# Optimization experiments

Hardware: AMD Instinct MI355X
Metric: run time of the kernel (lower is better)

The kernel has to match this reference:

```python
import jax, jax.numpy as jnp
import numpy as np

B, S, D_IN, D_OUT = 4, 2048, 1024, 1024

def setup_inputs() -> dict:
    key = jax.random.key(0)
    kx, kq, kk, kv = jax.random.split(key, 4)
    sc = 1.0 / np.sqrt(D_IN)
    x = jax.random.normal(kx, (B, S, D_IN), dtype=jnp.float32)
    Wq = jax.random.normal(kq, (D_IN, D_OUT), dtype=jnp.float32) * sc
    Wk = jax.random.normal(kk, (D_IN, D_OUT), dtype=jnp.float32) * sc
    Wv = jax.random.normal(kv, (D_IN, D_OUT), dtype=jnp.float32) * sc
    return {"x": x, "Wq": Wq, "Wk": Wk, "Wv": Wv}

def reference(x, Wq, Wk, Wv):
    # x: [B,S,Din]; projections to [B,S,Dout]
    q = jnp.einsum('bsd,de->bse', x, Wq)
    k = jnp.einsum('bsd,de->bse', x, Wk)
    v = jnp.einsum('bsd,de->bse', x, Wv)
    scale = 1.0 / jnp.sqrt(jnp.asarray(q.shape[-1], q.dtype))
    scores = jnp.einsum('bqe,bke->bqk', q, k) * scale  # [B,S,S]
    causal = jnp.tril(jnp.ones((scores.shape[-2], scores.shape[-1]), dtype=bool))
    scores = jnp.where(causal, scores, -jnp.inf)
    attn = jax.nn.softmax(scores, axis=-1)
    # dropout p=0.0 -> identity
    return jnp.einsum('bqk,bke->bqe', attn, v)
```

## Files before the change

### kernel.cpp

```cpp
#include <hip/hip_runtime.h>

#define SEQ 2048
#define DIM 1024

typedef __attribute__((ext_vector_type(8))) __bf16 bf16x8;
typedef __attribute__((ext_vector_type(4))) float f32x4;

typedef __attribute__((address_space(1))) unsigned char gu8_t;
typedef __attribute__((address_space(3))) unsigned char lu8_t;

__device__ __forceinline__ void async_copy16(const void* g, void* l) {
  __builtin_amdgcn_global_load_lds((gu8_t*)g, (lu8_t*)l, 16, 0, 0);
}

__device__ __forceinline__ ushort f2bf(float f) {
  union { float f; unsigned u; } v;
  v.f = f;
  unsigned r = v.u + 0x7FFFu + ((v.u >> 16) & 1u);
  return (ushort)(r >> 16);
}

__global__ void prep(const void* __restrict__ xin, const void* __restrict__ w0,
                     const void* __restrict__ w1, const void* __restrict__ w2,
                     ushort* __restrict__ xb, ushort* __restrict__ wt,
                     int* __restrict__ flag, float* __restrict__ lsum) {
  __shared__ ushort tile[64][68];
  __shared__ int redi[4];
  const int bid = blockIdx.x;
  const int t = threadIdx.x;

  const unsigned* words = (const unsigned*)xin;
  int hits = 0;
#pragma unroll
  for (int i = 0; i < 4; i++) {
    const unsigned wv = words[t * 4 + i];
    const unsigned b = (wv >> 8) & 0x7Fu;
    hits += (b >= 0x3Bu && b <= 0x42u) ? 1 : 0;
  }
#pragma unroll
  for (int o = 32; o > 0; o >>= 1) hits += __shfl_xor(hits, o, 64);
  if ((t & 63) == 0) redi[t >> 6] = hits;
  __syncthreads();
  const int bf = (redi[0] + redi[1] + redi[2] + redi[3] > 512) ? 1 : 0;

  if (bid >= 1792) {
    reinterpret_cast<float4*>(lsum)[(bid - 1792) * 256 + t] =
        make_float4(0.f, 0.f, 0.f, 0.f);
    if (bid == 1792 && t == 0) *flag = bf;
    return;
  }

  if (bid < 1024) {
#pragma unroll
    for (int j = 0; j < 4; j++) {
      const int i = bid * 1024 + j * 256 + t;
      if (bf) {
        reinterpret_cast<uint4*>(xb)[i] =
            reinterpret_cast<const uint4*>(xin)[i];
      } else {
        const float4* f = reinterpret_cast<const float4*>(xin);
        const float4 a = f[2 * i], b = f[2 * i + 1];
        ushort4 lo, hi;
        lo.x = f2bf(a.x); lo.y = f2bf(a.y); lo.z = f2bf(a.z); lo.w = f2bf(a.w);
        hi.x = f2bf(b.x); hi.y = f2bf(b.y); hi.z = f2bf(b.z); hi.w = f2bf(b.w);
        reinterpret_cast<ushort4*>(xb)[2 * i] = lo;
        reinterpret_cast<ushort4*>(xb)[2 * i + 1] = hi;
      }
    }
    return;
  }

  const int rem = bid - 1024;
  const int z = rem >> 8;
  const int within = rem & 255;
  const int c0 = (within & 15) * 64, r0 = (within >> 4) * 64;
  const void* in = (z == 0) ? w0 : (z == 1) ? w1 : w2;
  ushort* op = wt + (size_t)z * 1024 * 1024;

  if (bf) {
    const ushort* ip = (const ushort*)in;
#pragma unroll
    for (int i = 0; i < 4; i++) {
      const int lin = i * 256 + t;
      const int r = lin >> 4, c4 = (lin & 15) << 2;
      const ushort4 v = *reinterpret_cast<const ushort4*>(
          ip + (size_t)(r0 + r) * 1024 + c0 + c4);
      tile[r][c4 + 0] = v.x; tile[r][c4 + 1] = v.y;
      tile[r][c4 + 2] = v.z; tile[r][c4 + 3] = v.w;
    }
  } else {
    const float* ip = (const float*)in;
#pragma unroll
    for (int i = 0; i < 4; i++) {
      const int lin = i * 256 + t;
      const int r = lin >> 4, c4 = (lin & 15) << 2;
      const float4 v = *reinterpret_cast<const float4*>(
          ip + (size_t)(r0 + r) * 1024 + c0 + c4);
      tile[r][c4 + 0] = f2bf(v.x); tile[r][c4 + 1] = f2bf(v.y);
      tile[r][c4 + 2] = f2bf(v.z); tile[r][c4 + 3] = f2bf(v.w);
    }
  }
  __syncthreads();
#pragma unroll
  for (int i = 0; i < 4; i++) {
    const int lin = i * 256 + t;
    const int c = lin >> 4, r4 = (lin & 15) << 2;
    ushort4 v;
    v.x = tile[r4 + 0][c]; v.y = tile[r4 + 1][c];
    v.z = tile[r4 + 2][c]; v.w = tile[r4 + 3][c];
    *reinterpret_cast<ushort4*>(op + (size_t)(c0 + c) * 1024 + r0 + r4) = v;
  }
}

template <int MODE>
__global__ __launch_bounds__(512, 2) void gemm8(
    const ushort* __restrict__ p0, const ushort* __restrict__ p1,
    const ushort* __restrict__ p2, void* __restrict__ c0,
    void* __restrict__ c1, float* __restrict__ lsum) {
  __shared__ ushort sA[2][2][128 * 64];
  __shared__ ushort sB[2][2][128 * 64];

  const ushort* A;
  const ushort* B;
  ushort* C;
  float* ls = nullptr;
  int m0, n0;
  long ldA, ldB, ldC;
  float scale = 1.0f;
  bool isE = false;

  const int id = blockIdx.x;
  if constexpr (MODE == 0) {
    const int z = id >> 7, r = id & 127;
    m0 = (r >> 2) << 8;
    n0 = (r & 3) << 8;
    A = p0; ldA = 1024;
    B = p1 + (size_t)z * 1024 * 1024; ldB = 1024;
    C = (ushort*)c0 + (size_t)z * 8192 * 1024; ldC = 1024;
    scale = z ? 1.0f : 0.03125f;
  } else {
    if (id < 144) {
      isE = true;
      const int z = id / 36;
      const int tri = id % 36;
      int mt = 0;
      while ((mt + 1) * (mt + 2) / 2 <= tri) mt++;
      const int nt = tri - mt * (mt + 1) / 2;
      m0 = mt << 8;
      n0 = nt << 8;
      A = p0 + (size_t)z * SEQ * DIM; ldA = 1024;
      B = p0 + (size_t)8192 * 1024 + (size_t)z * SEQ * DIM; ldB = 1024;
      C = (ushort*)c0 + (size_t)z * SEQ * SEQ; ldC = 2048;
      ls = lsum + (size_t)z * SEQ;
    } else {
      const int r = id - 144;
      m0 = (r >> 5) << 8;
      n0 = (r & 31) << 8;
      A = p1 + 2 * 1024 * 1024; ldA = 1024;
      B = p2; ldB = 1024;
      C = (ushort*)c1; ldC = 8192;
    }
  }
  const int nT = 16;

  const int tid = threadIdx.x;
  const int lane = tid & 63;
  const int w = tid >> 6;
  const int quad = lane >> 4;
  const int l15 = lane & 15;
  const int ah = w >> 2;
  const int wn = (w & 3) << 6;
  const int bh = wn >> 7;
  const int bo = wn & 64;

  const ushort* aSrc[2][2];
  const ushort* bSrc[2][2];
#pragma unroll
  for (int h = 0; h < 2; h++)
#pragma unroll
    for (int i = 0; i < 2; i++) {
      const int g = i * 512 + tid;
      const int rl = g >> 3;
      const int ck = (g & 7) ^ (rl & 7);
      aSrc[h][i] = A + (size_t)(m0 + h * 128 + rl) * ldA + ck * 8;
      bSrc[h][i] = B + (size_t)(n0 + h * 128 + rl) * ldB + ck * 8;
    }

  auto stageA = [&](int t, int b) {
#pragma unroll
    for (int h = 0; h < 2; h++)
#pragma unroll
      for (int i = 0; i < 2; i++)
        async_copy16(aSrc[h][i] + t * 64, &sA[b][h][(i * 512 + tid) * 8]);
  };
  auto stageB = [&](int t, int b) {
#pragma unroll
    for (int h = 0; h < 2; h++)
#pragma unroll
      for (int i = 0; i < 2; i++)
        async_copy16(bSrc[h][i] + t * 64, &sB[b][h][(i * 512 + tid) * 8]);
  };
  auto rdA = [&](int b, int rbase, int kh) -> bf16x8 {
    const int row = rbase + l15;
    const int ck = ((kh << 2) | quad) ^ (row & 7);
    return *(const bf16x8*)&sA[b][ah][row * 64 + ck * 8];
  };
  auto rdB = [&](int b, int rbase, int kh) -> bf16x8 {
    const int row = rbase + l15;
    const int ck = ((kh << 2) | quad) ^ (row & 7);
    return *(const bf16x8*)&sB[b][bh][row * 64 + ck * 8];
  };

  f32x4 acc[8][4] = {};
  bf16x8 aF[8], bF0[4], bF1[4];

  stageA(0, 0); stageB(0, 0);
  stageA(1, 1); stageB(1, 1);
  asm volatile("s_waitcnt vmcnt(8)" ::: "memory");
  __builtin_amdgcn_s_barrier();

#pragma unroll 1
  for (int t = 0; t < nT; t++) {
    const int b = t & 1;

#pragma unroll
    for (int m = 0; m < 4; m++)
#pragma unroll
      for (int h = 0; h < 2; h++) aF[m * 2 + h] = rdA(b, m * 16, h);
#pragma unroll
    for (int n = 0; n < 2; n++)
#pragma unroll
      for (int h = 0; h < 2; h++) bF0[n * 2 + h] = rdB(b, bo + n * 16, h);
    __builtin_amdgcn_s_barrier();
    __builtin_amdgcn_s_setprio(1);
#pragma unroll
    for (int h = 0; h < 2; h++)
#pragma unroll
      for (int m = 0; m < 4; m++)
#pragma unroll
        for (int n = 0; n < 2; n++)
          acc[m][n] = __builtin_amdgcn_mfma_f32_16x16x32_bf16(
              aF[m * 2 + h], bF0[n * 2 + h], acc[m][n], 0, 0, 0);
    __builtin_amdgcn_s_setprio(0);
    __builtin_amdgcn_s_barrier();

#pragma unroll
    for (int n = 0; n < 2; n++)
#pragma unroll
      for (int h = 0; h < 2; h++)
        bF1[n * 2 + h] = rdB(b, bo + 32 + n * 16, h);
    __builtin_amdgcn_s_barrier();
    __builtin_amdgcn_s_setprio(1);
#pragma unroll
    for (int h = 0; h < 2; h++)
#pragma unroll
      for (int m = 0; m < 4; m++)
#pragma unroll
        for (int n = 0; n < 2; n++)
          acc[m][2 + n] = __builtin_amdgcn_mfma_f32_16x16x32_bf16(
              aF[m * 2 + h], bF1[n * 2 + h], acc[m][2 + n], 0, 0, 0);
    __builtin_amdgcn_s_setprio(0);
    __builtin_amdgcn_s_barrier();

#pragma unroll
    for (int m = 0; m < 4; m++)
#pragma unroll
      for (int h = 0; h < 2; h++) aF[m * 2 + h] = rdA(b, 64 + m * 16, h);
    if (t + 2 < nT) stageB(t + 2, b);
    __builtin_amdgcn_s_barrier();
    __builtin_amdgcn_s_setprio(1);
#pragma unroll
    for (int h = 0; h < 2; h++)
#pragma unroll
      for (int m = 0; m < 4; m++)
#pragma unroll
        for (int n = 0; n < 2; n++)
          acc[4 + m][n] = __builtin_amdgcn_mfma_f32_16x16x32_bf16(
              aF[m * 2 + h], bF0[n * 2 + h], acc[4 + m][n], 0, 0, 0);
    __builtin_amdgcn_s_setprio(0);
    __builtin_amdgcn_s_barrier();

    if (t + 2 < nT) stageA(t + 2, b);
    __builtin_amdgcn_s_setprio(1);
#pragma unroll
    for (int h = 0; h < 2; h++)
#pragma unroll
      for (int m = 0; m < 4; m++)
#pragma unroll
        for (int n = 0; n < 2; n++)
          acc[4 + m][2 + n] = __builtin_amdgcn_mfma_f32_16x16x32_bf16(
              aF[m * 2 + h], bF1[n * 2 + h], acc[4 + m][2 + n], 0, 0, 0);
    __builtin_amdgcn_s_setprio(0);
    if (t + 2 < nT)
      asm volatile("s_waitcnt vmcnt(8)" ::: "memory");
    else
      asm volatile("s_waitcnt vmcnt(0)" ::: "memory");
    __builtin_amdgcn_s_barrier();
  }

  if (MODE == 1 && isE) {
#pragma unroll
    for (int mi = 0; mi < 8; mi++)
#pragma unroll
      for (int r = 0; r < 4; r++) {
        const int row = m0 + ah * 128 + mi * 16 + quad * 4 + r;
        float partial = 0.0f;
#pragma unroll
        for (int ni = 0; ni < 4; ni++) {
          const int col = n0 + wn + ni * 16 + l15;
          const float ev = (col <= row) ? __expf(acc[mi][ni][r]) : 0.0f;
          C[(size_t)row * ldC + col] = f2bf(ev);
          partial += ev;
        }
#pragma unroll
        for (int o = 1; o < 16; o <<= 1) partial += __shfl_xor(partial, o, 64);
        if (l15 == 0) atomicAdd(&ls[row], partial);
      }
  } else {
#pragma unroll
    for (int mi = 0; mi < 8; mi++)
#pragma unroll
      for (int ni = 0; ni < 4; ni++)
#pragma unroll
        for (int r = 0; r < 4; r++) {
          const int row = m0 + ah * 128 + mi * 16 + quad * 4 + r;
          const int col = n0 + wn + ni * 16 + l15;
          C[(size_t)row * ldC + col] = f2bf(acc[mi][ni][r] * scale);
        }
  }
}

template <int EPI, int OUTK, int CK, int SWIZ, int M, int N, int K, long AZ,
          long BZ, long CZ, long BRS>
__global__ __launch_bounds__(256, 4) void gemm_t(
    const ushort* __restrict__ A, const ushort* __restrict__ Bt,
    void* __restrict__ Cv, const int* __restrict__ flag,
    float* __restrict__ lsum, float scale0, float scale1) {
  __shared__ ushort lA[128 * 64];
  __shared__ ushort lB[128 * 64];
  __shared__ float lsh[(EPI == 2) ? 128 : 1];

  constexpr int MT = M / 128;
  const int nT = gridDim.x;
  const int id = blockIdx.y * nT + blockIdx.x;
  const int xcd = id & 7;
  const int loc = id >> 3;
  int nt, mt;
  if constexpr (SWIZ == 1) {
    const int ng = nT >> 3;
    nt = xcd * ng + loc % ng;
    mt = loc / ng;
  } else if constexpr (SWIZ == 2) {
    if (loc <= xcd) { mt = xcd; nt = loc; }
    else { mt = MT - 1 - xcd; nt = loc - xcd - 1; }
  } else if constexpr (SWIZ == 3) {
    nt = xcd;
    mt = loc;
  } else {
    nt = loc % nT;
    mt = xcd + ((loc / nT) << 3);
  }
  const int n0 = nt * 128;
  const int m0 = mt * 128;

  const int z = blockIdx.z;
  const ushort* Ab = A + (size_t)z * AZ;
  const ushort* Bb = Bt + (size_t)z * BZ;

  const int t = threadIdx.x;
  const int lane = t & 63;
  const int w = t >> 6;
  const int wm = (w >> 1) * 64;
  const int wn = (w & 1) * 64;
  const int quad = lane >> 4;
  const int l15 = lane & 15;

  if constexpr (EPI == 2) {
    if (t < 128) lsh[t] = 1.0f / lsum[(size_t)z * M + m0 + t];
  }

  f32x4 acc[4][4] = {};

  const int kEnd = CK ? ((m0 + 128 < K) ? (m0 + 128) : K) : K;

  for (int k0 = 0; k0 < kEnd; k0 += 64) {
    __syncthreads();
#pragma unroll
    for (int g0 = 0; g0 < 1024; g0 += 256) {
      const int g = g0 + t;
      const int r = g >> 3, c = (g & 7) << 3;
      async_copy16(Ab + (size_t)(m0 + r) * K + k0 + c, lA + g * 8);
    }
#pragma unroll
    for (int g0 = 0; g0 < 1024; g0 += 256) {
      const int g = g0 + t;
      const int r = g >> 3, c = (g & 7) << 3;
      async_copy16(Bb + (size_t)(n0 + r) * BRS + k0 + c, lB + g * 8);
    }
    __syncthreads();

#pragma unroll
    for (int h = 0; h < 2; h++) {
      bf16x8 af[4], bfr[4];
#pragma unroll
      for (int mi = 0; mi < 4; mi++)
        af[mi] = *(const bf16x8*)(lA + (wm + mi * 16 + l15) * 64 + h * 32 +
                                  quad * 8);
#pragma unroll
      for (int ni = 0; ni < 4; ni++)
        bfr[ni] = *(const bf16x8*)(lB + (wn + ni * 16 + l15) * 64 + h * 32 +
                                   quad * 8);
#pragma unroll
      for (int mi = 0; mi < 4; mi++)
#pragma unroll
        for (int ni = 0; ni < 4; ni++)
          acc[mi][ni] = __builtin_amdgcn_mfma_f32_16x16x32_bf16(
              af[mi], bfr[ni], acc[mi][ni], 0, 0, 0);
    }
  }

  const size_t zc = (size_t)z * CZ;

  if constexpr (EPI == 1) {
    ushort* C = (ushort*)Cv + zc;
    float* ls = lsum + (size_t)z * M;
#pragma unroll
    for (int mi = 0; mi < 4; mi++)
#pragma unroll
      for (int r = 0; r < 4; r++) {
        const int row = m0 + wm + mi * 16 + quad * 4 + r;
        float partial = 0.0f;
#pragma unroll
        for (int ni = 0; ni < 4; ni++) {
          const int col = n0 + wn + ni * 16 + l15;
          const float ev = (col <= row) ? __expf(acc[mi][ni][r]) : 0.0f;
          C[(size_t)row * N + col] = f2bf(ev);
          partial += ev;
        }
#pragma unroll
        for (int o = 1; o < 16; o <<= 1) partial += __shfl_xor(partial, o, 64);
        if (l15 == 0) atomicAdd(&ls[row], partial);
      }
    return;
  } else {
    const float scale = (z == 0) ? scale0 : scale1;
    const bool storeBf = (OUTK == 1) || (OUTK == 2 && *flag != 0);
#pragma unroll
    for (int mi = 0; mi < 4; mi++)
#pragma unroll
      for (int ni = 0; ni < 4; ni++)
#pragma unroll
        for (int r = 0; r < 4; r++) {
          const int lrow = wm + mi * 16 + quad * 4 + r;
          const int row = m0 + lrow;
          const int col = n0 + wn + ni * 16 + l15;
          const float sc = (EPI == 2) ? lsh[lrow] : scale;
          const float vv = acc[mi][ni][r] * sc;
          if (storeBf) {
            ushort* C = (ushort*)Cv + zc;
            C[(size_t)row * N + col] = f2bf(vv);
          } else {
            float* C = (float*)Cv + zc;
            C[(size_t)row * N + col] = vv;
          }
        }
  }
}

extern "C" void kernel_launch(void* const* d_in, const int* in_sizes, int n_in,
                              void* d_out, int out_size, void* d_ws,
                              size_t ws_size, hipStream_t stream) {
  char* ws = (char*)d_ws;
  const size_t MB = 1024 * 1024;
  int* flag = (int*)ws;
  ushort* wt = (ushort*)(ws + 1 * MB);
  ushort* xb = (ushort*)(ws + 7 * MB);
  ushort* q = (ushort*)(ws + 23 * MB);
  ushort* vt = (ushort*)(ws + 55 * MB);
  ushort* sc = (ushort*)(ws + 71 * MB);
  float* lsum = (float*)(ws + 103 * MB);

  prep<<<dim3(1800), 256, 0, stream>>>(d_in[0], d_in[1], d_in[2], d_in[3], xb,
                                       wt, flag, lsum);

  gemm8<0><<<dim3(256), 512, 0, stream>>>(xb, wt, nullptr, (void*)q, nullptr,
                                          nullptr);

  gemm8<1><<<dim3(272), 512, 0, stream>>>(q, wt, xb, (void*)sc, (void*)vt,
                                          lsum);

  gemm_t<2, 2, 1, 3, 2048, 1024, 2048, (long)SEQ * SEQ, 2048L,
         (long)SEQ * DIM, 8192L>
      <<<dim3(8, 16, 4), 256, 0, stream>>>(sc, vt, d_out, flag, lsum, 1.0f,
                                           1.0f);
}
```

Measured before the change: 241.6 us.

## Replace P·V gemm with split-K 256x256 gemm8 mode using atomic fp32 accumulation

The final attention-times-V GEMM now runs on the larger pipelined 256x256 gemm8 kernel instead of the simpler 128x128 gemm_t. The causal K range is split into balanced chunks through a packed lookup table, giving 60 blocks per batch. Each block scales its partial result by the inverse row sum and atomically adds it into a zeroed fp32 output. This improves tile reuse and load balance across the triangular work, at the cost of an extra memset, atomic adds to global memory, and dropping the bf16 output path that the flag used to select.

```diff
diff --git a/kernel.cpp b/kernel.cpp
--- a/kernel.cpp
+++ b/kernel.cpp
@@ -122,10 +122,13 @@
 
   const ushort* A;
   const ushort* B;
-  ushort* C;
+  ushort* C = nullptr;
+  float* Cf = nullptr;
   float* ls = nullptr;
   int m0, n0;
-  long ldA, ldB, ldC;
+  int k0 = 0;
+  int nTloc = 16;
+  long ldA, ldB, ldC = 0;
   float scale = 1.0f;
   bool isE = false;
 
@@ -138,7 +141,7 @@
     B = p1 + (size_t)z * 1024 * 1024; ldB = 1024;
     C = (ushort*)c0 + (size_t)z * 8192 * 1024; ldC = 1024;
     scale = z ? 1.0f : 0.03125f;
-  } else {
+  } else if constexpr (MODE == 1) {
     if (id < 144) {
       isE = true;
       const int z = id / 36;
@@ -160,8 +163,26 @@
       B = p2; ldB = 1024;
       C = (ushort*)c1; ldC = 8192;
     }
-  }
-  const int nT = 16;
+  } else {
+    const int z = id / 60;
+    const int rr = id % 60;
+    const int nt = rr / 15;
+    const int u = rr % 15;
+    const unsigned long long lut0 = 0x855C845343824100ULL;
+    const unsigned long long lut1 = 0x00779F876E5E869DULL;
+    const unsigned bb =
+        (unsigned)((u < 8 ? (lut0 >> (8 * u)) : (lut1 >> (8 * (u - 8)))) &
+                   0xFFull);
+    const int mt = bb & 7;
+    k0 = ((bb >> 3) & 7) << 8;
+    nTloc = (int)((bb >> 6) + 1) << 2;
+    m0 = mt << 8;
+    n0 = nt << 8;
+    A = p0 + (size_t)z * SEQ * SEQ; ldA = 2048;
+    B = p1 + (size_t)z * SEQ; ldB = 8192;
+    Cf = (float*)c0 + (size_t)z * SEQ * DIM;
+    ls = lsum + (size_t)z * SEQ;
+  }
 
   const int tid = threadIdx.x;
   const int lane = tid & 63;
@@ -182,8 +203,8 @@
       const int g = i * 512 + tid;
       const int rl = g >> 3;
       const int ck = (g & 7) ^ (rl & 7);
-      aSrc[h][i] = A + (size_t)(m0 + h * 128 + rl) * ldA + ck * 8;
-      bSrc[h][i] = B + (size_t)(n0 + h * 128 + rl) * ldB + ck * 8;
+      aSrc[h][i] = A + (size_t)(m0 + h * 128 + rl) * ldA + k0 + ck * 8;
+      bSrc[h][i] = B + (size_t)(n0 + h * 128 + rl) * ldB + k0 + ck * 8;
     }
 
   auto stageA = [&](int t, int b) {
@@ -220,7 +241,7 @@
   __builtin_amdgcn_s_barrier();
 
 #pragma unroll 1
-  for (int t = 0; t < nT; t++) {
+  for (int t = 0; t < nTloc; t++) {
     const int b = t & 1;
 
 #pragma unroll
@@ -266,7 +287,7 @@
     for (int m = 0; m < 4; m++)
 #pragma unroll
       for (int h = 0; h < 2; h++) aF[m * 2 + h] = rdA(b, 64 + m * 16, h);
-    if (t + 2 < nT) stageB(t + 2, b);
+    if (t + 2 < nTloc) stageB(t + 2, b);
     __builtin_amdgcn_s_barrier();
     __builtin_amdgcn_s_setprio(1);
 #pragma unroll
@@ -280,7 +301,7 @@
     __builtin_amdgcn_s_setprio(0);
     __builtin_amdgcn_s_barrier();
 
-    if (t + 2 < nT) stageA(t + 2, b);
+    if (t + 2 < nTloc) stageA(t + 2, b);
     __builtin_amdgcn_s_setprio(1);
 #pragma unroll
     for (int h = 0; h < 2; h++)
@@ -291,11 +312,31 @@
           acc[4 + m][2 + n] = __builtin_amdgcn_mfma_f32_16x16x32_bf16(
               aF[m * 2 + h], bF1[n * 2 + h], acc[4 + m][2 + n], 0, 0, 0);
     __builtin_amdgcn_s_setprio(0);
-    if (t + 2 < nT)
+    if (t + 2 < nTloc)
       asm volatile("s_waitcnt vmcnt(8)" ::: "memory");
     else
       asm volatile("s_waitcnt vmcnt(0)" ::: "memory");
     __builtin_amdgcn_s_barrier();
+  }
+
+  if constexpr (MODE == 2) {
+    __syncthreads();
+    float* lshp = (float*)(&sA[0][0][0]);
+    if (tid < 256) lshp[tid] = 1.0f / ls[m0 + tid];
+    __syncthreads();
+#pragma unroll
+    for (int mi = 0; mi < 8; mi++)
+#pragma unroll
+      for (int ni = 0; ni < 4; ni++)
+#pragma unroll
+        for (int r = 0; r < 4; r++) {
+          const int rl_ = ah * 128 + mi * 16 + quad * 4 + r;
+          const int row = m0 + rl_;
+          const int col = n0 + wn + ni * 16 + l15;
+          atomicAdd(&Cf[(size_t)row * DIM + col],
+                    acc[mi][ni][r] * lshp[rl_]);
+        }
+    return;
   }
 
   if (MODE == 1 && isE) {
@@ -326,143 +367,6 @@
           const int row = m0 + ah * 128 + mi * 16 + quad * 4 + r;
           const int col = n0 + wn + ni * 16 + l15;
           C[(size_t)row * ldC + col] = f2bf(acc[mi][ni][r] * scale);
-        }
-  }
-}
-
-template <int EPI, int OUTK, int CK, int SWIZ, int M, int N, int K, long AZ,
-          long BZ, long CZ, long BRS>
-__global__ __launch_bounds__(256, 4) void gemm_t(
-    const ushort* __restrict__ A, const ushort* __restrict__ Bt,
-    void* __restrict__ Cv, const int* __restrict__ flag,
-    float* __restrict__ lsum, float scale0, float scale1) {
-  __shared__ ushort lA[128 * 64];
-  __shared__ ushort lB[128 * 64];
-  __shared__ float lsh[(EPI == 2) ? 128 : 1];
-
-  constexpr int MT = M / 128;
-  const int nT = gridDim.x;
-  const int id = blockIdx.y * nT + blockIdx.x;
-  const int xcd = id & 7;
-  const int loc = id >> 3;
-  int nt, mt;
-  if constexpr (SWIZ == 1) {
-    const int ng = nT >> 3;
-    nt = xcd * ng + loc % ng;
-    mt = loc / ng;
-  } else if constexpr (SWIZ == 2) {
-    if (loc <= xcd) { mt = xcd; nt = loc; }
-    else { mt = MT - 1 - xcd; nt = loc - xcd - 1; }
-  } else if constexpr (SWIZ == 3) {
-    nt = xcd;
-    mt = loc;
-  } else {
-    nt = loc % nT;
-    mt = xcd + ((loc / nT) << 3);
-  }
-  const int n0 = nt * 128;
-  const int m0 = mt * 128;
-
-  const int z = blockIdx.z;
-  const ushort* Ab = A + (size_t)z * AZ;
-  const ushort* Bb = Bt + (size_t)z * BZ;
-
-  const int t = threadIdx.x;
-  const int lane = t & 63;
-  const int w = t >> 6;
-  const int wm = (w >> 1) * 64;
-  const int wn = (w & 1) * 64;
-  const int quad = lane >> 4;
-  const int l15 = lane & 15;
-
-  if constexpr (EPI == 2) {
-    if (t < 128) lsh[t] = 1.0f / lsum[(size_t)z * M + m0 + t];
-  }
-
-  f32x4 acc[4][4] = {};
-
-  const int kEnd = CK ? ((m0 + 128 < K) ? (m0 + 128) : K) : K;
-
-  for (int k0 = 0; k0 < kEnd; k0 += 64) {
-    __syncthreads();
-#pragma unroll
-    for (int g0 = 0; g0 < 1024; g0 += 256) {
-      const int g = g0 + t;
-      const int r = g >> 3, c = (g & 7) << 3;
-      async_copy16(Ab + (size_t)(m0 + r) * K + k0 + c, lA + g * 8);
-    }
-#pragma unroll
-    for (int g0 = 0; g0 < 1024; g0 += 256) {
-      const int g = g0 + t;
-      const int r = g >> 3, c = (g & 7) << 3;
-      async_copy16(Bb + (size_t)(n0 + r) * BRS + k0 + c, lB + g * 8);
-    }
-    __syncthreads();
-
-#pragma unroll
-    for (int h = 0; h < 2; h++) {
-      bf16x8 af[4], bfr[4];
-#pragma unroll
-      for (int mi = 0; mi < 4; mi++)
-        af[mi] = *(const bf16x8*)(lA + (wm + mi * 16 + l15) * 64 + h * 32 +
-                                  quad * 8);
-#pragma unroll
-      for (int ni = 0; ni < 4; ni++)
-        bfr[ni] = *(const bf16x8*)(lB + (wn + ni * 16 + l15) * 64 + h * 32 +
-                                   quad * 8);
-#pragma unroll
-      for (int mi = 0; mi < 4; mi++)
-#pragma unroll
-        for (int ni = 0; ni < 4; ni++)
-          acc[mi][ni] = __builtin_amdgcn_mfma_f32_16x16x32_bf16(
-              af[mi], bfr[ni], acc[mi][ni], 0, 0, 0);
-    }
-  }
-
-  const size_t zc = (size_t)z * CZ;
-
-  if constexpr (EPI == 1) {
-    ushort* C = (ushort*)Cv + zc;
-    float* ls = lsum + (size_t)z * M;
-#pragma unroll
-    for (int mi = 0; mi < 4; mi++)
-#pragma unroll
-      for (int r = 0; r < 4; r++) {
-        const int row = m0 + wm + mi * 16 + quad * 4 + r;
-        float partial = 0.0f;
-#pragma unroll
-        for (int ni = 0; ni < 4; ni++) {
-          const int col = n0 + wn + ni * 16 + l15;
-          const float ev = (col <= row) ? __expf(acc[mi][ni][r]) : 0.0f;
-          C[(size_t)row * N + col] = f2bf(ev);
-          partial += ev;
-        }
-#pragma unroll
-        for (int o = 1; o < 16; o <<= 1) partial += __shfl_xor(partial, o, 64);
-        if (l15 == 0) atomicAdd(&ls[row], partial);
-      }
-    return;
-  } else {
-    const float scale = (z == 0) ? scale0 : scale1;
-    const bool storeBf = (OUTK == 1) || (OUTK == 2 && *flag != 0);
-#pragma unroll
-    for (int mi = 0; mi < 4; mi++)
-#pragma unroll
-      for (int ni = 0; ni < 4; ni++)
-#pragma unroll
-        for (int r = 0; r < 4; r++) {
-          const int lrow = wm + mi * 16 + quad * 4 + r;
-          const int row = m0 + lrow;
-          const int col = n0 + wn + ni * 16 + l15;
-          const float sc = (EPI == 2) ? lsh[lrow] : scale;
-          const float vv = acc[mi][ni][r] * sc;
-          if (storeBf) {
-            ushort* C = (ushort*)Cv + zc;
-            C[(size_t)row * N + col] = f2bf(vv);
-          } else {
-            float* C = (float*)Cv + zc;
-            C[(size_t)row * N + col] = vv;
-          }
         }
   }
 }
@@ -480,6 +384,8 @@
   ushort* sc = (ushort*)(ws + 71 * MB);
   float* lsum = (float*)(ws + 103 * MB);
 
+  hipMemsetAsync(d_out, 0, (size_t)4 * SEQ * DIM * sizeof(float), stream);
+
   prep<<<dim3(1800), 256, 0, stream>>>(d_in[0], d_in[1], d_in[2], d_in[3], xb,
                                        wt, flag, lsum);
 
@@ -489,8 +395,6 @@
   gemm8<1><<<dim3(272), 512, 0, stream>>>(q, wt, xb, (void*)sc, (void*)vt,
                                           lsum);
 
-  gemm_t<2, 2, 1, 3, 2048, 1024, 2048, (long)SEQ * SEQ, 2048L,
-         (long)SEQ * DIM, 8192L>
-      <<<dim3(8, 16, 4), 256, 0, stream>>>(sc, vt, d_out, flag, lsum, 1.0f,
-                                           1.0f);
+  gemm8<2><<<dim3(240), 512, 0, stream>>>(sc, vt, nullptr, d_out, nullptr,
+                                          lsum);
 }
```

Measured after the change: 263.0 us. 1.09x slower.

## Prefetch all LDS fragments per k-tile before MFMA phases and drop precomputed source pointers

Applied to the files above, without the earlier changes.

All A and B fragments for a k-tile (low and high A halves plus both B halves) are now read from LDS right after the first barrier. This overlaps the later LDS reads with the first MFMA phase and removes one barrier and the mid-loop read stalls. The eight precomputed global source pointers are replaced by one base pointer per matrix plus constant offsets, which frees registers. The cost is higher VGPR pressure from holding 24 bf16x8 fragments at once, which could reduce occupancy or cause spills.

```diff
diff --git a/kernel.cpp b/kernel.cpp
--- a/kernel.cpp
+++ b/kernel.cpp
@@ -161,7 +161,7 @@
       C = (ushort*)c1; ldC = 8192;
     }
   }
-  const int nT = 16;
+  constexpr int nT = 16;
 
   const int tid = threadIdx.x;
   const int lane = tid & 63;
@@ -173,32 +173,26 @@
   const int bh = wn >> 7;
   const int bo = wn & 64;
 
-  const ushort* aSrc[2][2];
-  const ushort* bSrc[2][2];
-#pragma unroll
-  for (int h = 0; h < 2; h++)
-#pragma unroll
-    for (int i = 0; i < 2; i++) {
-      const int g = i * 512 + tid;
-      const int rl = g >> 3;
-      const int ck = (g & 7) ^ (rl & 7);
-      aSrc[h][i] = A + (size_t)(m0 + h * 128 + rl) * ldA + ck * 8;
-      bSrc[h][i] = B + (size_t)(n0 + h * 128 + rl) * ldB + ck * 8;
-    }
+  const int rl0 = tid >> 3;
+  const int ck0 = (tid & 7) ^ (rl0 & 7);
+  const ushort* aBase = A + (size_t)(m0 + rl0) * ldA + ck0 * 8;
+  const ushort* bBase = B + (size_t)(n0 + rl0) * ldB + ck0 * 8;
 
   auto stageA = [&](int t, int b) {
 #pragma unroll
     for (int h = 0; h < 2; h++)
 #pragma unroll
       for (int i = 0; i < 2; i++)
-        async_copy16(aSrc[h][i] + t * 64, &sA[b][h][(i * 512 + tid) * 8]);
+        async_copy16(aBase + (size_t)(h * 128 + i * 64) * ldA + t * 64,
+                     &sA[b][h][(i * 512 + tid) * 8]);
   };
   auto stageB = [&](int t, int b) {
 #pragma unroll
     for (int h = 0; h < 2; h++)
 #pragma unroll
       for (int i = 0; i < 2; i++)
-        async_copy16(bSrc[h][i] + t * 64, &sB[b][h][(i * 512 + tid) * 8]);
+        async_copy16(bBase + (size_t)(h * 128 + i * 64) * ldB + t * 64,
+                     &sB[b][h][(i * 512 + tid) * 8]);
   };
   auto rdA = [&](int b, int rbase, int kh) -> bf16x8 {
     const int row = rbase + l15;
@@ -212,7 +206,7 @@
   };
 
   f32x4 acc[8][4] = {};
-  bf16x8 aF[8], bF0[4], bF1[4];
+  bf16x8 aLo[8], aHi[8], bF0[4], bF1[4];
 
   stageA(0, 0); stageB(0, 0);
   stageA(1, 1); stageB(1, 1);
@@ -226,12 +220,23 @@
 #pragma unroll
     for (int m = 0; m < 4; m++)
 #pragma unroll
-      for (int h = 0; h < 2; h++) aF[m * 2 + h] = rdA(b, m * 16, h);
+      for (int h = 0; h < 2; h++) aLo[m * 2 + h] = rdA(b, m * 16, h);
 #pragma unroll
     for (int n = 0; n < 2; n++)
 #pragma unroll
       for (int h = 0; h < 2; h++) bF0[n * 2 + h] = rdB(b, bo + n * 16, h);
     __builtin_amdgcn_s_barrier();
+
+#pragma unroll
+    for (int m = 0; m < 4; m++)
+#pragma unroll
+      for (int h = 0; h < 2; h++) aHi[m * 2 + h] = rdA(b, 64 + m * 16, h);
+#pragma unroll
+    for (int n = 0; n < 2; n++)
+#pragma unroll
+      for (int h = 0; h < 2; h++)
+        bF1[n * 2 + h] = rdB(b, bo + 32 + n * 16, h);
+
     __builtin_amdgcn_s_setprio(1);
 #pragma unroll
     for (int h = 0; h < 2; h++)
@@ -240,16 +245,10 @@
 #pragma unroll
         for (int n = 0; n < 2; n++)
           acc[m][n] = __builtin_amdgcn_mfma_f32_16x16x32_bf16(
-              aF[m * 2 + h], bF0[n * 2 + h], acc[m][n], 0, 0, 0);
+              aLo[m * 2 + h], bF0[n * 2 + h], acc[m][n], 0, 0, 0);
     __builtin_amdgcn_s_setprio(0);
     __builtin_amdgcn_s_barrier();
 
-#pragma unroll
-    for (int n = 0; n < 2; n++)
-#pragma unroll
-      for (int h = 0; h < 2; h++)
-        bF1[n * 2 + h] = rdB(b, bo + 32 + n * 16, h);
-    __builtin_amdgcn_s_barrier();
     __builtin_amdgcn_s_setprio(1);
 #pragma unroll
     for (int h = 0; h < 2; h++)
@@ -258,16 +257,13 @@
 #pragma unroll
         for (int n = 0; n < 2; n++)
           acc[m][2 + n] = __builtin_amdgcn_mfma_f32_16x16x32_bf16(
-              aF[m * 2 + h], bF1[n * 2 + h], acc[m][2 + n], 0, 0, 0);
+              aLo[m * 2 + h], bF1[n * 2 + h], acc[m][2 + n], 0, 0, 0);
     __builtin_amdgcn_s_setprio(0);
     __builtin_amdgcn_s_barrier();
 
-#pragma unroll
-    for (int m = 0; m < 4; m++)
-#pragma unroll
-      for (int h = 0; h < 2; h++) aF[m * 2 + h] = rdA(b, 64 + m * 16, h);
     if (t + 2 < nT) stageB(t + 2, b);
     __builtin_amdgcn_s_barrier();
+
     __builtin_amdgcn_s_setprio(1);
 #pragma unroll
     for (int h = 0; h < 2; h++)
@@ -276,7 +272,7 @@
 #pragma unroll
         for (int n = 0; n < 2; n++)
           acc[4 + m][n] = __builtin_amdgcn_mfma_f32_16x16x32_bf16(
-              aF[m * 2 + h], bF0[n * 2 + h], acc[4 + m][n], 0, 0, 0);
+              aHi[m * 2 + h], bF0[n * 2 + h], acc[4 + m][n], 0, 0, 0);
     __builtin_amdgcn_s_setprio(0);
     __builtin_amdgcn_s_barrier();
 
@@ -289,7 +285,7 @@
 #pragma unroll
         for (int n = 0; n < 2; n++)
           acc[4 + m][2 + n] = __builtin_amdgcn_mfma_f32_16x16x32_bf16(
-              aF[m * 2 + h], bF1[n * 2 + h], acc[4 + m][2 + n], 0, 0, 0);
+              aHi[m * 2 + h], bF1[n * 2 + h], acc[4 + m][2 + n], 0, 0, 0);
     __builtin_amdgcn_s_setprio(0);
     if (t + 2 < nT)
       asm volatile("s_waitcnt vmcnt(8)" ::: "memory");
```

After: 244.1 us. Within noise of the previous version (+1.1%).
